# Kernel tuning notes

Hardware: AMD Instinct MI355X
Metric: run time of the kernel (lower is better)

Reference implementation:

```python
import jax, jax.numpy as jnp
import numpy as np

N = 200000
E = 200000
X_SIZE = 256
H_SIZE = 256


def setup_inputs() -> dict:
    key = jax.random.key(0)
    ks = jax.random.split(key, 8)
    s = 1.0 / np.sqrt(H_SIZE)
    return {
        "x": jax.random.normal(ks[0], (N, X_SIZE), jnp.float32),
        "h": jax.random.normal(ks[1], (N, H_SIZE), jnp.float32),
        "c": jax.random.normal(ks[2], (N, H_SIZE), jnp.float32),
        "src": jax.random.randint(ks[3], (E,), 0, N),
        "dst": jax.random.randint(ks[4], (E,), 0, N),
        "W_iou": jax.random.normal(ks[5], (3 * H_SIZE, X_SIZE), jnp.float32) * s,
        "U_iou": jax.random.normal(ks[6], (3 * H_SIZE, H_SIZE), jnp.float32) * s,
        "b_iou": jnp.zeros((1, 3 * H_SIZE), jnp.float32),
        "U_f_w": jax.random.normal(ks[7], (H_SIZE, H_SIZE), jnp.float32) * s,
        "U_f_b": jnp.zeros((H_SIZE,), jnp.float32),
    }


def reference(x, h, c, src, dst, W_iou, U_iou, b_iou, U_f_w, U_f_b):
    # message + reduce (mode='sum'): ragged segment-sum of child states per parent
    h_sum = jax.ops.segment_sum(h[src], dst, num_segments=N)  # [N, H]
    c_sum = jax.ops.segment_sum(c[src], dst, num_segments=N)  # [N, H]
    # forget gate on aggregated child hidden state
    f = jax.nn.sigmoid(h_sum @ U_f_w.T + U_f_b)               # [N, H]
    c_red = f * c_sum
    # apply_node_func: iou = W_iou(x) (leaf init) + U_iou(h_sum) + b_iou
    iou = x @ W_iou.T + h_sum @ U_iou.T + b_iou               # [N, 3H]
    i, o, u = jnp.split(iou, 3, axis=1)
    c_new = jax.nn.sigmoid(i) * jnp.tanh(u) + c_red
    h_new = jax.nn.sigmoid(o) * jnp.tanh(c_new)
    return h_new, c_new
```

## Files before the change

kernel.cpp:

```cpp
#include <hip/hip_runtime.h>
#include <hip/hip_bf16.h>
#include <stdint.h>

#define NN 200000
#define EE 200000
#define NB 196

__device__ __forceinline__ short f2bf(float f) {
  union { float f; unsigned u; } a; a.f = f;
  unsigned r = a.u + 0x7fffu + ((a.u >> 16) & 1u);
  return (short)(r >> 16);
}
__device__ __forceinline__ int pack2bf(float a, float b) {
  return (int)(((unsigned)(unsigned short)f2bf(a)) | ((unsigned)(unsigned short)f2bf(b) << 16));
}
__device__ __forceinline__ float bf2f(unsigned short s) {
  union { float f; unsigned u; } a; a.u = ((unsigned)s) << 16;
  return a.f;
}
__device__ __forceinline__ float sigm(float x) { return 1.f / (1.f + __expf(-x)); }
__device__ __forceinline__ float tanh_fast(float x) {
  x = fminf(fmaxf(x, -15.f), 15.f);
  float e = __expf(2.f * x);
  return (e - 1.f) / (e + 1.f);
}

using bf16x8 = __attribute__((ext_vector_type(8))) short;
using f32x4  = __attribute__((ext_vector_type(4))) float;

__device__ __forceinline__ void load_lds16(const void* g, void* l) {
  __builtin_amdgcn_global_load_lds((const __attribute__((address_space(1))) void*)g,
                                   (__attribute__((address_space(3))) void*)l, 16, 0, 0);
}

__global__ void count_kernel(const int* __restrict__ dst, int* __restrict__ counts) {
  int e = blockIdx.x * 256 + threadIdx.x;
  if (e < EE) atomicAdd(counts + dst[e], 1);
}

__global__ void scan_sums(const int* __restrict__ counts, int* __restrict__ bsum) {
  __shared__ int lds[256];
  int t = threadIdx.x, b = blockIdx.x;
  int base = b * 1024 + t * 4, s = 0;
#pragma unroll
  for (int i = 0; i < 4; ++i) { int idx = base + i; if (idx < NN) s += counts[idx]; }
  lds[t] = s; __syncthreads();
  for (int off = 128; off > 0; off >>= 1) {
    if (t < off) lds[t] += lds[t + off];
    __syncthreads();
  }
  if (t == 0) bsum[b] = lds[0];
}

__global__ void scan_blocks(const int* __restrict__ bsum, int* __restrict__ boff) {
  __shared__ int lds[256];
  int t = threadIdx.x;
  int v = (t < NB) ? bsum[t] : 0;
  lds[t] = v; __syncthreads();
  for (int off = 1; off < 256; off <<= 1) {
    int add = (t >= off) ? lds[t - off] : 0;
    __syncthreads();
    lds[t] += add;
    __syncthreads();
  }
  if (t < NB) boff[t] = lds[t] - v;
}

__global__ void scan_offsets(const int* __restrict__ counts, const int* __restrict__ boff,
                             int* __restrict__ offs) {
  __shared__ int lds[256];
  int t = threadIdx.x, b = blockIdx.x;
  int base = b * 1024 + t * 4;
  int c0 = (base     < NN) ? counts[base]     : 0;
  int c1 = (base + 1 < NN) ? counts[base + 1] : 0;
  int c2 = (base + 2 < NN) ? counts[base + 2] : 0;
  int c3 = (base + 3 < NN) ? counts[base + 3] : 0;
  int s = c0 + c1 + c2 + c3;
  lds[t] = s; __syncthreads();
  for (int off = 1; off < 256; off <<= 1) {
    int add = (t >= off) ? lds[t - off] : 0;
    __syncthreads();
    lds[t] += add;
    __syncthreads();
  }
  int run = boff[b] + lds[t] - s;
  if (base     < NN) offs[base]     = run; run += c0;
  if (base + 1 < NN) offs[base + 1] = run; run += c1;
  if (base + 2 < NN) offs[base + 2] = run; run += c2;
  if (base + 3 < NN) offs[base + 3] = run;
}

__global__ void fill_kernel(const int* __restrict__ src, const int* __restrict__ dst,
                            const int* __restrict__ offs, int* __restrict__ cursor,
                            int* __restrict__ eidx) {
  int e = blockIdx.x * 256 + threadIdx.x;
  if (e < EE) {
    int d = dst[e];
    int p = offs[d] + atomicAdd(cursor + d, 1);
    eidx[p] = src[e];
  }
}

__global__ void gather_pack(const float* __restrict__ x, const float* __restrict__ h,
                            const float* __restrict__ c, const int* __restrict__ offs,
                            const int* __restrict__ eidx, short* __restrict__ A,
                            float* __restrict__ csum) {
  int gid = blockIdx.x * 256 + threadIdx.x;
  int n = gid >> 6, l = gid & 63;
  int beg = offs[n];
  int end = (n == NN - 1) ? EE : offs[n + 1];
  float4 hs = {0.f, 0.f, 0.f, 0.f};
  float4 cs = {0.f, 0.f, 0.f, 0.f};
  for (int k = beg; k < end; ++k) {
    int s = eidx[k];
    const float4 hv = *(const float4*)(h + (size_t)s * 256 + l * 4);
    const float4 cv = *(const float4*)(c + (size_t)s * 256 + l * 4);
    hs.x += hv.x; hs.y += hv.y; hs.z += hv.z; hs.w += hv.w;
    cs.x += cv.x; cs.y += cv.y; cs.z += cv.z; cs.w += cv.w;
  }
  *(float4*)(csum + (size_t)n * 256 + l * 4) = cs;
  const float4 xv = *(const float4*)(x + (size_t)n * 256 + l * 4);
  int2 xo, ho;
  xo.x = pack2bf(xv.x, xv.y); xo.y = pack2bf(xv.z, xv.w);
  ho.x = pack2bf(hs.x, hs.y); ho.y = pack2bf(hs.z, hs.w);
  *(int2*)(A + (size_t)n * 512 + l * 4)       = xo;
  *(int2*)(A + (size_t)n * 512 + 256 + l * 4) = ho;
}

__global__ void pack_b_kernel(const float* __restrict__ W_iou, const float* __restrict__ U_iou,
                              const float* __restrict__ b_iou, const float* __restrict__ U_f_w,
                              const float* __restrict__ U_f_b,
                              short* __restrict__ Bp, float* __restrict__ biasp) {
  int idx = blockIdx.x * 256 + threadIdx.x;
  if (idx >= 1024 * 512) return;
  int p = idx >> 9, k = idx & 511;
  int j = p >> 2, comp = p & 3;
  float v;
  if (comp < 3) v = (k < 256) ? W_iou[(size_t)(comp * 256 + j) * 256 + k]
                              : U_iou[(size_t)(comp * 256 + j) * 256 + (k - 256)];
  else          v = (k < 256) ? 0.f : U_f_w[(size_t)j * 256 + (k - 256)];
  Bp[(size_t)p * 512 + k] = f2bf(v);
  if (k == 0) biasp[p] = (comp < 3) ? b_iou[comp * 256 + j] : U_f_b[j];
}

__global__ __launch_bounds__(256)
void gemm_fused(const short* __restrict__ A, const short* __restrict__ Bp,
                const float* __restrict__ biasp,
                float* __restrict__ outh, float* __restrict__ outc) {
  __shared__ short smem[16384];
  short* sA = smem;
  short* sB = smem + 8192;

  const int tid  = threadIdx.x;
  const int lane = tid & 63;
  const int wave = tid >> 6;
  const int wm = wave >> 1, wn = wave & 1;
  const int row16 = lane & 15, quad = lane >> 4;

  const int mbase = blockIdx.y * 128;
  const int nbase = blockIdx.x * 128;
  const int wbase = wave * 64;

  f32x4 acc[4][4];
#pragma unroll
  for (int i = 0; i < 4; ++i)
#pragma unroll
    for (int j = 0; j < 4; ++j)
      acc[i][j] = (f32x4){0.f, 0.f, 0.f, 0.f};

  for (int kt = 0; kt < 512; kt += 64) {
#pragma unroll
    for (int i = 0; i < 4; ++i) {
      int s = i * 256 + tid;
      int r = s >> 3, seg = s & 7;
      int ra = mbase + r; if (ra > NN - 1) ra = NN - 1;
      const short* gA = A  + (size_t)ra * 512 + kt + seg * 8;
      const short* gB = Bp + (size_t)(nbase + r) * 512 + kt + seg * 8;
      load_lds16(gA, sA + (i * 256 + wbase) * 8);
      load_lds16(gB, sB + (i * 256 + wbase) * 8);
    }
    __syncthreads();
#pragma unroll
    for (int kk = 0; kk < 64; kk += 32) {
      bf16x8 af[4], bfr[4];
#pragma unroll
      for (int mi = 0; mi < 4; ++mi)
        af[mi] = *(const bf16x8*)(sA + (wm * 64 + mi * 16 + row16) * 64 + kk + quad * 8);
#pragma unroll
      for (int ni = 0; ni < 4; ++ni)
        bfr[ni] = *(const bf16x8*)(sB + (wn * 64 + ni * 16 + row16) * 64 + kk + quad * 8);
#pragma unroll
      for (int mi = 0; mi < 4; ++mi)
#pragma unroll
        for (int ni = 0; ni < 4; ++ni)
          acc[mi][ni] = __builtin_amdgcn_mfma_f32_16x16x32_bf16(af[mi], bfr[ni], acc[mi][ni], 0, 0, 0);
    }
    __syncthreads();
  }

  float biasv[4];
#pragma unroll
  for (int ni = 0; ni < 4; ++ni)
    biasv[ni] = biasp[nbase + wn * 64 + ni * 16 + row16];

  short* Y = smem;
#pragma unroll
  for (int mi = 0; mi < 4; ++mi)
#pragma unroll
    for (int ni = 0; ni < 4; ++ni)
#pragma unroll
      for (int r = 0; r < 4; ++r) {
        int lrow = wm * 64 + mi * 16 + quad * 4 + r;
        int lcol = wn * 64 + ni * 16 + row16;
        Y[lrow * 128 + lcol] = f2bf(acc[mi][ni][r] + biasv[ni]);
      }
  __syncthreads();

  const int jbase = nbase >> 2;
#pragma unroll
  for (int t = 0; t < 16; ++t) {
    int u2 = t * 256 + tid;
    int row = u2 >> 5, jj = u2 & 31;
    int grow = mbase + row;
    if (grow < NN) {
      const unsigned short* yp = (const unsigned short*)Y + row * 128 + jj * 4;
      ushort4 y4 = *(const ushort4*)yp;
      float iv = bf2f(y4.x), ov = bf2f(y4.y), uv = bf2f(y4.z), fv = bf2f(y4.w);
      size_t off = (size_t)grow * 256 + (jbase + jj);
      float csum = outc[off];
      float cnew = sigm(iv) * tanh_fast(uv) + sigm(fv) * csum;
      float hnew = sigm(ov) * tanh_fast(cnew);
      outh[off] = hnew;
      outc[off] = cnew;
    }
  }
}

extern "C" void kernel_launch(void* const* d_in, const int* in_sizes, int n_in,
                              void* d_out, int out_size, void* d_ws, size_t ws_size,
                              hipStream_t stream) {
  const float* x     = (const float*)d_in[0];
  const float* h     = (const float*)d_in[1];
  const float* c     = (const float*)d_in[2];
  const int*   src   = (const int*)d_in[3];
  const int*   dst   = (const int*)d_in[4];
  const float* W_iou = (const float*)d_in[5];
  const float* U_iou = (const float*)d_in[6];
  const float* b_iou = (const float*)d_in[7];
  const float* U_f_w = (const float*)d_in[8];
  const float* U_f_b = (const float*)d_in[9];

  float* outh = (float*)d_out;
  float* outc = outh + (size_t)NN * 256;

  short* A     = (short*)d_ws;
  short* Bp    = A + (size_t)NN * 512;
  float* biasp = (float*)(Bp + 1024 * 512);

  int* scratch = (int*)d_out;
  int* counts  = scratch;
  int* cursor  = scratch + NN;
  int* eidx    = scratch + 2 * NN;
  int* offs    = scratch + 2 * NN + EE;
  int* bsum    = scratch + 3 * NN + EE;
  int* boff    = bsum + NB;

  hipMemsetAsync(scratch, 0, (size_t)(2 * NN) * sizeof(int), stream);

  count_kernel <<<(EE + 255) / 256, 256, 0, stream>>>(dst, counts);
  scan_sums    <<<NB, 256, 0, stream>>>(counts, bsum);
  scan_blocks  <<<1, 256, 0, stream>>>(bsum, boff);
  scan_offsets <<<NB, 256, 0, stream>>>(counts, boff, offs);
  fill_kernel  <<<(EE + 255) / 256, 256, 0, stream>>>(src, dst, offs, cursor, eidx);
  gather_pack  <<<(NN * 64) / 256, 256, 0, stream>>>(x, h, c, offs, eidx, A, outc);
  pack_b_kernel<<<(1024 * 512) / 256, 256, 0, stream>>>(W_iou, U_iou, b_iou, U_f_w, U_f_b, Bp, biasp);
  gemm_fused   <<<dim3(8, 1563), 256, 0, stream>>>(A, Bp, biasp, outh, outc);
}
```

Measured before the change: 1.428 ms.

## Double-buffer GEMM LDS tiles, swizzle LDS layout, and remap blocks per XCD

Measured after the change: 1.299 ms. 9.0% less time.

```diff
diff --git a/kernel.cpp b/kernel.cpp
--- a/kernel.cpp
+++ b/kernel.cpp
@@ -147,18 +147,24 @@
 void gemm_fused(const short* __restrict__ A, const short* __restrict__ Bp,
                 const float* __restrict__ biasp,
                 float* __restrict__ outh, float* __restrict__ outc) {
-  __shared__ short smem[16384];
-  short* sA = smem;
-  short* sB = smem + 8192;
+  __shared__ short smem[32768];
 
   const int tid  = threadIdx.x;
   const int lane = tid & 63;
   const int wave = tid >> 6;
   const int wm = wave >> 1, wn = wave & 1;
   const int row16 = lane & 15, quad = lane >> 4;
-
-  const int mbase = blockIdx.y * 128;
-  const int nbase = blockIdx.x * 128;
+  const int rx = row16 & 7;
+
+  const int lin = blockIdx.x;
+  const int xcd = lin & 7;
+  const int t8  = lin >> 3;
+  const int mp  = xcd * 196 + (t8 >> 3);
+  const int nb  = t8 & 7;
+  const int mbase = mp * 128;
+  const int nbase = nb * 128;
+  if (mbase >= NN) return;
+
   const int wbase = wave * 64;
 
   f32x4 acc[4][4];
@@ -168,40 +174,70 @@
     for (int j = 0; j < 4; ++j)
       acc[i][j] = (f32x4){0.f, 0.f, 0.f, 0.f};
 
-  for (int kt = 0; kt < 512; kt += 64) {
-#pragma unroll
-    for (int i = 0; i < 4; ++i) {
-      int s = i * 256 + tid;
-      int r = s >> 3, seg = s & 7;
-      int ra = mbase + r; if (ra > NN - 1) ra = NN - 1;
-      const short* gA = A  + (size_t)ra * 512 + kt + seg * 8;
-      const short* gB = Bp + (size_t)(nbase + r) * 512 + kt + seg * 8;
-      load_lds16(gA, sA + (i * 256 + wbase) * 8);
-      load_lds16(gB, sB + (i * 256 + wbase) * 8);
+  float biasv[4];
+#pragma unroll
+  for (int ni = 0; ni < 4; ++ni) {
+    biasv[ni] = biasp[nbase + wn * 64 + ni * 16 + row16];
+    asm volatile("" :: "v"(biasv[ni]));
+  }
+
+  const short* gAb[4];
+  const short* gBb[4];
+#pragma unroll
+  for (int i = 0; i < 4; ++i) {
+    int s = i * 256 + tid;
+    int r = s >> 3, seg = s & 7;
+    int sseg = seg ^ (r & 7);
+    int ra = mbase + r; if (ra > NN - 1) ra = NN - 1;
+    gAb[i] = A  + (size_t)ra * 512 + sseg * 8;
+    gBb[i] = Bp + (size_t)(nbase + r) * 512 + sseg * 8;
+  }
+
+#pragma unroll
+  for (int i = 0; i < 4; ++i) {
+    load_lds16(gAb[i], smem + (i * 256 + wbase) * 8);
+    load_lds16(gBb[i], smem + 8192 + (i * 256 + wbase) * 8);
+  }
+
+  for (int t = 0; t < 8; ++t) {
+    if (t < 7) {
+      const int kt = (t + 1) * 64;
+      short* db = smem + ((t + 1) & 1) * 16384;
+#pragma unroll
+      for (int i = 0; i < 4; ++i) {
+        load_lds16(gAb[i] + kt, db + (i * 256 + wbase) * 8);
+        load_lds16(gBb[i] + kt, db + 8192 + (i * 256 + wbase) * 8);
+      }
+      asm volatile("s_waitcnt vmcnt(8)" ::: "memory");
+    } else {
+      asm volatile("s_waitcnt vmcnt(0)" ::: "memory");
     }
-    __syncthreads();
+    __builtin_amdgcn_sched_barrier(0);
+    __builtin_amdgcn_s_barrier();
+    __builtin_amdgcn_sched_barrier(0);
+
+    const short* sAc = smem + (t & 1) * 16384;
+    const short* sBc = sAc + 8192;
 #pragma unroll
     for (int kk = 0; kk < 64; kk += 32) {
+      const int K8 = kk >> 3;
       bf16x8 af[4], bfr[4];
 #pragma unroll
       for (int mi = 0; mi < 4; ++mi)
-        af[mi] = *(const bf16x8*)(sA + (wm * 64 + mi * 16 + row16) * 64 + kk + quad * 8);
+        af[mi] = *(const bf16x8*)(sAc + (wm * 64 + mi * 16 + row16) * 64 + (((K8 + quad) ^ rx)) * 8);
 #pragma unroll
       for (int ni = 0; ni < 4; ++ni)
-        bfr[ni] = *(const bf16x8*)(sB + (wn * 64 + ni * 16 + row16) * 64 + kk + quad * 8);
+        bfr[ni] = *(const bf16x8*)(sBc + (wn * 64 + ni * 16 + row16) * 64 + (((K8 + quad) ^ rx)) * 8);
 #pragma unroll
       for (int mi = 0; mi < 4; ++mi)
 #pragma unroll
         for (int ni = 0; ni < 4; ++ni)
           acc[mi][ni] = __builtin_amdgcn_mfma_f32_16x16x32_bf16(af[mi], bfr[ni], acc[mi][ni], 0, 0, 0);
     }
-    __syncthreads();
-  }
-
-  float biasv[4];
-#pragma unroll
-  for (int ni = 0; ni < 4; ++ni)
-    biasv[ni] = biasp[nbase + wn * 64 + ni * 16 + row16];
+    __builtin_amdgcn_sched_barrier(0);
+    __builtin_amdgcn_s_barrier();
+    __builtin_amdgcn_sched_barrier(0);
+  }
 
   short* Y = smem;
 #pragma unroll
@@ -274,5 +310,5 @@
   fill_kernel  <<<(EE + 255) / 256, 256, 0, stream>>>(src, dst, offs, cursor, eidx);
   gather_pack  <<<(NN * 64) / 256, 256, 0, stream>>>(x, h, c, offs, eidx, A, outc);
   pack_b_kernel<<<(1024 * 512) / 256, 256, 0, stream>>>(W_iou, U_iou, b_iou, U_f_w, U_f_b, Bp, biasp);
-  gemm_fused   <<<dim3(8, 1563), 256, 0, stream>>>(A, Bp, biasp, outh, outc);
-}
+  gemm_fused   <<<8 * 196 * 8, 256, 0, stream>>>(A, Bp, biasp, outh, outc);
+}
```
